# Kernel optimization log

Hardware: AMD Instinct MI355X
Metric: run time of the kernel (lower is better)

## Reference

```python
import jax, jax.numpy as jnp
import numpy as np

def setup_inputs() -> dict:
    key = jax.random.key(0)
    k1, k2, k3, k4, k5 = jax.random.split(key, 5)
    B, Lc, Lq, D = 32, 512, 64, 1024
    return {
        "c": jax.random.normal(k1, (B, Lc, D), dtype=jnp.float32),
        "q": jax.random.normal(k2, (B, Lq, D), dtype=jnp.float32),
        "proj_c": jax.random.normal(k3, (D, 1), dtype=jnp.float32) * 0.04,
        "proj_q": jax.random.normal(k4, (D, 1), dtype=jnp.float32) * 0.04,
        "proj_cq": jax.random.normal(k5, (1, 1, D), dtype=jnp.float32) * 0.04,
    }

def reference(c, q, proj_c, proj_q, proj_cq):
    # similarity: s0 + s1 + s2, shape [B, Lc, Lq]
    s0 = c @ proj_c                                   # [B, Lc, 1]
    s1 = jnp.swapaxes(q @ proj_q, 1, 2)               # [B, 1, Lq]
    s2 = jnp.einsum('bcd,bqd->bcq', c * proj_cq, q)   # [B, Lc, Lq]
    sim = s0 + s1 + s2

    # context-to-query attention
    a_c2q = jax.nn.softmax(sim, axis=-1)              # [B, Lc, Lq]
    c2q = jnp.einsum('bcq,bqd->bcd', a_c2q, q)        # [B, Lc, D]

    # query-to-context attention (max over query dim, softmax over context)
    a_q2c = jax.nn.softmax(jnp.max(sim, axis=-1), axis=-1)  # [B, Lc]
    q2c = jnp.einsum('bc,bcd->bd', a_q2c, c)[:, None, :]    # [B, 1, D], broadcasts over Lc

    out = jnp.concatenate((c, c2q, c * q2c, c * c2q), axis=-1)  # [B, Lc, 4D]
    return out
```

## Files before the change

kernel.cpp:

```cpp
#include <hip/hip_runtime.h>

#define B 32
#define LC 512
#define LQ 64
#define DD 1024


typedef __attribute__((ext_vector_type(8))) short bf16x8;
typedef __attribute__((ext_vector_type(4))) float f32x4;

__device__ inline short f2bf(float f) {
    unsigned u = __builtin_bit_cast(unsigned, f);
    u += 0x7FFFu + ((u >> 16) & 1u);
    return (short)(u >> 16);
}

__device__ inline bf16x8 pack8(float4 a, float4 b) {
    bf16x8 r;
    r[0] = f2bf(a.x); r[1] = f2bf(a.y); r[2] = f2bf(a.z); r[3] = f2bf(a.w);
    r[4] = f2bf(b.x); r[5] = f2bf(b.y); r[6] = f2bf(b.z); r[7] = f2bf(b.w);
    return r;
}

__device__ inline float dot4(float4 a, float4 b) {
    return a.x * b.x + a.y * b.y + a.z * b.z + a.w * b.w;
}

__device__ inline int xswz(int bid, int nwg) {
    return (bid & 7) * (nwg >> 3) + (bid >> 3);
}

__global__ __launch_bounds__(256) void k0_q(const float* __restrict__ q,
                                            const float* __restrict__ proj_q,
                                            short* __restrict__ qbf,
                                            short* __restrict__ qT,
                                            float* __restrict__ s1part) {
    const int bid = xswz(blockIdx.x, 512);
    const int b  = bid >> 4;
    const int d0 = (bid & 15) * 64;
    const int sl = bid & 15;
    const int t  = threadIdx.x;

    __shared__ __align__(16) short tile[64][72];
    __shared__ float s1red[64][8];

    const int j0 = (t & 31) * 2;
    const int dg = t >> 5;

    const float* qr0 = q + (size_t)(b * LQ + j0) * DD + d0 + dg * 8;
    const float* qr1 = qr0 + DD;
    float4 x0 = *(const float4*)(qr0 + 0);
    float4 x1 = *(const float4*)(qr0 + 4);
    float4 y0 = *(const float4*)(qr1 + 0);
    float4 y1 = *(const float4*)(qr1 + 4);
    float4 p0 = *(const float4*)(proj_q + d0 + dg * 8);
    float4 p1 = *(const float4*)(proj_q + d0 + dg * 8 + 4);

    s1red[j0][dg]     = dot4(x0, p0) + dot4(x1, p1);
    s1red[j0 + 1][dg] = dot4(y0, p0) + dot4(y1, p1);

    *(bf16x8*)&qbf[(size_t)(b * LQ + j0) * DD + d0 + dg * 8]     = pack8(x0, x1);
    *(bf16x8*)&qbf[(size_t)(b * LQ + j0 + 1) * DD + d0 + dg * 8] = pack8(y0, y1);

    const float* fx0 = (const float*)&x0;
    const float* fx1 = (const float*)&x1;
    const float* fy0 = (const float*)&y0;
    const float* fy1 = (const float*)&y1;
#pragma unroll
    for (int e = 0; e < 8; ++e) {
        float v0 = (e < 4) ? fx0[e] : fx1[e - 4];
        float v1 = (e < 4) ? fy0[e] : fy1[e - 4];
        unsigned pk = (unsigned)(unsigned short)f2bf(v0)
                    | ((unsigned)(unsigned short)f2bf(v1) << 16);
        *(unsigned*)&tile[dg * 8 + e][j0] = pk;
    }
    __syncthreads();

    {
        const int d = t >> 2, part = t & 3;
        bf16x8 v0 = *(const bf16x8*)&tile[d][part * 16];
        bf16x8 v1 = *(const bf16x8*)&tile[d][part * 16 + 8];
        short* dst = qT + ((size_t)b * DD + d0 + d) * LQ + part * 16;
        *(bf16x8*)(dst)     = v0;
        *(bf16x8*)(dst + 8) = v1;
    }
    if (t < 64) {
        float s = 0.f;
#pragma unroll
        for (int k = 0; k < 8; ++k) s += s1red[t][k];
        s1part[(b * 16 + sl) * 64 + t] = s;
    }
}

__global__ __launch_bounds__(256) void k1_sim(const float* __restrict__ c,
                                              const short* __restrict__ qbf,
                                              const float* __restrict__ proj_c,
                                              const float* __restrict__ proj_cq,
                                              const float* __restrict__ s1part,
                                              short* __restrict__ P,
                                              float* __restrict__ mfull) {
    const int bid = xswz(blockIdx.x, 512);
    const int b  = bid >> 4;
    const int i0 = (bid & 15) * 32;
    const int t  = threadIdx.x;
    const int w  = t >> 6, lane = t & 63;
    const int l15 = lane & 15, quad = lane >> 4;

    __shared__ __align__(16) short sA[32][72];
    __shared__ __align__(16) short sB[64][72];
    __shared__ float rmaxL[32][4];
    __shared__ float rsumL[32][4];
    __shared__ float s0red[32][8];
    __shared__ float s1L[64];

    const int arow = t >> 3, ag = t & 7;
    const int brow = t >> 2, bg = t & 3;

    const float* cbase = c + (size_t)(b * LC + i0 + arow) * DD + ag * 8;
    const short* qbase = qbf + (size_t)(b * LQ + brow) * DD + bg * 16;

    f32x4 acc[2] = {{0.f,0.f,0.f,0.f},{0.f,0.f,0.f,0.f}};
    float s0p = 0.f;

    float4 a0 = *(const float4*)(cbase + 0);
    float4 a1 = *(const float4*)(cbase + 4);
    bf16x8 u0 = *(const bf16x8*)(qbase + 0);
    bf16x8 u1 = *(const bf16x8*)(qbase + 8);

    for (int kc = 0; kc < 16; ++kc) {
        float4 na0, na1;
        bf16x8 nu0, nu1;
        if (kc < 15) {
            const float* cn = cbase + (kc + 1) * 64;
            const short* qn = qbase + (kc + 1) * 64;
            na0 = *(const float4*)(cn + 0);
            na1 = *(const float4*)(cn + 4);
            nu0 = *(const bf16x8*)(qn + 0);
            nu1 = *(const bf16x8*)(qn + 8);
        }
        {
            const float* pcq = proj_cq + kc * 64 + ag * 8;
            const float* pc  = proj_c  + kc * 64 + ag * 8;
            float4 p0 = *(const float4*)(pcq + 0);
            float4 p1 = *(const float4*)(pcq + 4);
            float4 c0 = *(const float4*)(pc + 0);
            float4 c1 = *(const float4*)(pc + 4);
            s0p += dot4(a0, c0) + dot4(a1, c1);
            float4 m0 = {a0.x * p0.x, a0.y * p0.y, a0.z * p0.z, a0.w * p0.w};
            float4 m1 = {a1.x * p1.x, a1.y * p1.y, a1.z * p1.z, a1.w * p1.w};
            *(bf16x8*)&sA[arow][ag * 8] = pack8(m0, m1);
            *(bf16x8*)&sB[brow][bg * 16 + 0] = u0;
            *(bf16x8*)&sB[brow][bg * 16 + 8] = u1;
        }
        __syncthreads();
#pragma unroll
        for (int s = 0; s < 2; ++s) {
            int ko = s * 32 + quad * 8;
            bf16x8 bf = *(const bf16x8*)&sB[w * 16 + l15][ko];
#pragma unroll
            for (int mt = 0; mt < 2; ++mt) {
                bf16x8 af = *(const bf16x8*)&sA[mt * 16 + l15][ko];
                acc[mt] = __builtin_amdgcn_mfma_f32_16x16x32_bf16(af, bf, acc[mt], 0, 0, 0);
            }
        }
        __syncthreads();
        if (kc < 15) { a0 = na0; a1 = na1; u0 = nu0; u1 = nu1; }
    }

    s0red[arow][ag] = s0p;
    if (t < 64) {
        float s = 0.f;
#pragma unroll
        for (int k = 0; k < 16; ++k) s += s1part[(b * 16 + k) * 64 + t];
        s1L[t] = s;
    }
    __syncthreads();

    const float s1j = s1L[w * 16 + l15];
    float v[2][4];
#pragma unroll
    for (int mt = 0; mt < 2; ++mt) {
#pragma unroll
        for (int r = 0; r < 4; ++r) {
            float vv = acc[mt][r] + s1j;
            v[mt][r] = vv;
            float rm = vv;
#pragma unroll
            for (int off = 1; off < 16; off <<= 1) rm = fmaxf(rm, __shfl_xor(rm, off, 16));
            if (l15 == 0) rmaxL[mt * 16 + quad * 4 + r][w] = rm;
        }
    }
    __syncthreads();
    float e[2][4];
#pragma unroll
    for (int mt = 0; mt < 2; ++mt) {
#pragma unroll
        for (int r = 0; r < 4; ++r) {
            int row = mt * 16 + quad * 4 + r;
            float m = fmaxf(fmaxf(rmaxL[row][0], rmaxL[row][1]),
                            fmaxf(rmaxL[row][2], rmaxL[row][3]));
            float ee = __expf(v[mt][r] - m);
            e[mt][r] = ee;
            float se = ee;
#pragma unroll
            for (int off = 1; off < 16; off <<= 1) se += __shfl_xor(se, off, 16);
            if (l15 == 0) rsumL[row][w] = se;
        }
    }
    __syncthreads();
#pragma unroll
    for (int mt = 0; mt < 2; ++mt) {
#pragma unroll
        for (int r = 0; r < 4; ++r) {
            int row = mt * 16 + quad * 4 + r;
            float s = rsumL[row][0] + rsumL[row][1] + rsumL[row][2] + rsumL[row][3];
            P[(size_t)(b * LC + i0 + row) * LQ + w * 16 + l15] = f2bf(e[mt][r] / s);
        }
    }
    if (t < 32) {
        float s0v = 0.f;
#pragma unroll
        for (int k = 0; k < 8; ++k) s0v += s0red[t][k];
        float mm = fmaxf(fmaxf(rmaxL[t][0], rmaxL[t][1]),
                         fmaxf(rmaxL[t][2], rmaxL[t][3]));
        mfull[b * LC + i0 + t] = mm + s0v;
    }
}

__global__ __launch_bounds__(256) void k2_q2c(const float* __restrict__ c,
                                              const float* __restrict__ mfull,
                                              float* __restrict__ q2c) {
    const int bid = xswz(blockIdx.x, 256);
    const int b  = bid >> 3;
    const int d0 = (bid & 7) * 128;
    const int t  = threadIdx.x;
    __shared__ float aL[LC];
    __shared__ float redm[4];
    __shared__ float reds[4];

    float m0 = mfull[b * LC + t];
    float m1 = mfull[b * LC + 256 + t];
    float mx = fmaxf(m0, m1);
#pragma unroll
    for (int off = 32; off; off >>= 1) mx = fmaxf(mx, __shfl_xor(mx, off, 64));
    if ((t & 63) == 0) redm[t >> 6] = mx;
    __syncthreads();
    float bm = fmaxf(fmaxf(redm[0], redm[1]), fmaxf(redm[2], redm[3]));
    float e0 = __expf(m0 - bm), e1 = __expf(m1 - bm);
    float s = e0 + e1;
#pragma unroll
    for (int off = 32; off; off >>= 1) s += __shfl_xor(s, off, 64);
    if ((t & 63) == 0) reds[t >> 6] = s;
    __syncthreads();
    float bs = reds[0] + reds[1] + reds[2] + reds[3];
    float inv = 1.0f / bs;
    aL[t] = e0 * inv;
    aL[t + 256] = e1 * inv;
    __syncthreads();

    const int tx = t & 31, ty = t >> 5;
    float4 acc = {0.f, 0.f, 0.f, 0.f};
    const float* cb = c + (size_t)b * LC * DD + d0 + tx * 4;
    for (int i = ty; i < LC; i += 8) {
        float a = aL[i];
        float4 cv = *(const float4*)(cb + (size_t)i * DD);
        acc.x += a * cv.x; acc.y += a * cv.y; acc.z += a * cv.z; acc.w += a * cv.w;
    }
    __shared__ __align__(16) float4 red[8][32];
    red[ty][tx] = acc;
    __syncthreads();
    if (t < 32) {
        float4 sv = red[0][t];
#pragma unroll
        for (int k = 1; k < 8; ++k) {
            float4 v2 = red[k][t];
            sv.x += v2.x; sv.y += v2.y; sv.z += v2.z; sv.w += v2.w;
        }
        *(float4*)(q2c + b * DD + d0 + t * 4) = sv;
    }
}

__global__ __launch_bounds__(256) void k3_out(const float* __restrict__ c,
                                              const short* __restrict__ qT,
                                              const short* __restrict__ P,
                                              const float* __restrict__ q2c,
                                              float* __restrict__ out) {
    const int bid = xswz(blockIdx.x, 2048);
    const int b  = bid >> 6;
    const int i0 = ((bid >> 2) & 15) * 32;
    const int qd = bid & 3;
    const int t  = threadIdx.x;
    const int w  = t >> 6, lane = t & 63;
    const int l15 = lane & 15, quad = lane >> 4;

    __shared__ __align__(16) short sBq[256][72];

    bf16x8 paf[2][2];
#pragma unroll
    for (int s = 0; s < 2; ++s)
#pragma unroll
        for (int mt = 0; mt < 2; ++mt)
            paf[s][mt] = *(const bf16x8*)&P[(size_t)(b * LC + i0 + mt * 16 + l15) * LQ
                                           + s * 32 + quad * 8];

    {
        const short* src = qT + ((size_t)b * DD + qd * 256) * LQ;
#pragma unroll
        for (int it = 0; it < 8; ++it) {
            int f = it * 256 + t;
            bf16x8 vv = *(const bf16x8*)(src + f * 8);
            *(bf16x8*)&sBq[f >> 3][(f & 7) * 8] = vv;
        }
    }
    __syncthreads();

    const float* cb  = c + (size_t)(b * LC + i0) * DD + qd * 256;
    const float* g2b = q2c + b * DD + qd * 256;
    float* ob = out + (size_t)(b * LC + i0) * (4 * DD) + qd * 256;

    for (int dci = 0; dci < 4; ++dci) {
        const int dl = dci * 64 + w * 16 + l15;
        float g2 = g2b[dl];
        f32x4 acc2[2] = {{0.f,0.f,0.f,0.f},{0.f,0.f,0.f,0.f}};
#pragma unroll
        for (int s = 0; s < 2; ++s) {
            bf16x8 bf = *(const bf16x8*)&sBq[dl][s * 32 + quad * 8];
#pragma unroll
            for (int mt = 0; mt < 2; ++mt)
                acc2[mt] = __builtin_amdgcn_mfma_f32_16x16x32_bf16(paf[s][mt], bf, acc2[mt], 0, 0, 0);
        }
#pragma unroll
        for (int mt = 0; mt < 2; ++mt) {
#pragma unroll
            for (int r = 0; r < 4; ++r) {
                int row = mt * 16 + quad * 4 + r;
                float cc = cb[(size_t)row * DD + dl];
                float cqv = acc2[mt][r];
                float* o = ob + (size_t)row * (4 * DD) + dl;
                o[0]      = cc;
                o[DD]     = cqv;
                o[2 * DD] = cc * g2;
                o[3 * DD] = cc * cqv;
            }
        }
    }
}

extern "C" void kernel_launch(void* const* d_in, const int* in_sizes, int n_in,
                              void* d_out, int out_size, void* d_ws, size_t ws_size,
                              hipStream_t stream) {
    const float* c       = (const float*)d_in[0];
    const float* q       = (const float*)d_in[1];
    const float* proj_c  = (const float*)d_in[2];
    const float* proj_q  = (const float*)d_in[3];
    const float* proj_cq = (const float*)d_in[4];
    float* out = (float*)d_out;
    float* ws  = (float*)d_ws;

    float* mfull  = ws;
    float* q2c    = ws + 16384;
    float* s1part = ws + 49152;
    short* P      = (short*)(ws + 81920);
    short* qbf    = (short*)(ws + 606208);
    short* qT     = (short*)(ws + 1654784);

    hipLaunchKernelGGL(k0_q,   dim3(512),  dim3(256), 0, stream, q, proj_q, qbf, qT, s1part);
    hipLaunchKernelGGL(k1_sim, dim3(512),  dim3(256), 0, stream,
                       c, qbf, proj_c, proj_cq, s1part, P, mfull);
    hipLaunchKernelGGL(k2_q2c, dim3(256),  dim3(256), 0, stream, c, mfull, q2c);
    hipLaunchKernelGGL(k3_out, dim3(2048), dim3(256), 0, stream, c, qT, P, q2c, out);
}
```

Measured before the change: 390.2 us.

## Double-buffer sim kernel, load MFMA B fragments directly, vectorize output stores

In the similarity kernel, the q bf16 B-fragments are now loaded straight from global memory into registers instead of staging them through shared memory. The A tile is double-buffered with a two-step prefetch, so each k-step needs one barrier instead of two. In the output kernel, the shared-memory staging of qT is removed and fragments are read directly from global memory. A 4x4 in-register transpose built from lane shuffles lets each lane issue float4 loads of c and float4 stores of all four output slices instead of scalar accesses. The trade-off is uncoalesced fragment loads from global memory and extra shuffle instructions in return for wider, better-coalesced output writes.

```diff
diff --git a/kernel.cpp b/kernel.cpp
--- a/kernel.cpp
+++ b/kernel.cpp
@@ -28,6 +28,20 @@
 
 __device__ inline int xswz(int bid, int nwg) {
     return (bid & 7) * (nwg >> 3) + (bid >> 3);
+}
+
+__device__ inline void xpose44(float v[4], int l15) {
+    const bool m0 = l15 & 1, m1 = l15 & 2;
+    float x0 = m0 ? v[0] : v[1];
+    float x1 = m0 ? v[2] : v[3];
+    x0 = __shfl_xor(x0, 1, 64);
+    x1 = __shfl_xor(x1, 1, 64);
+    if (m0) { v[0] = x0; v[2] = x1; } else { v[1] = x0; v[3] = x1; }
+    float y0 = m1 ? v[0] : v[2];
+    float y1 = m1 ? v[1] : v[3];
+    y0 = __shfl_xor(y0, 2, 64);
+    y1 = __shfl_xor(y1, 2, 64);
+    if (m1) { v[0] = y0; v[1] = y1; } else { v[2] = y0; v[3] = y1; }
 }
 
 __global__ __launch_bounds__(256) void k0_q(const float* __restrict__ q,
@@ -106,41 +120,64 @@
     const int w  = t >> 6, lane = t & 63;
     const int l15 = lane & 15, quad = lane >> 4;
 
-    __shared__ __align__(16) short sA[32][72];
-    __shared__ __align__(16) short sB[64][72];
+    __shared__ __align__(16) short sA[2][32][72];
     __shared__ float rmaxL[32][4];
     __shared__ float rsumL[32][4];
     __shared__ float s0red[32][8];
     __shared__ float s1L[64];
 
     const int arow = t >> 3, ag = t & 7;
-    const int brow = t >> 2, bg = t & 3;
 
     const float* cbase = c + (size_t)(b * LC + i0 + arow) * DD + ag * 8;
-    const short* qbase = qbf + (size_t)(b * LQ + brow) * DD + bg * 16;
+    const short* qfrag = qbf + (size_t)(b * LQ + w * 16 + l15) * DD + quad * 8;
 
     f32x4 acc[2] = {{0.f,0.f,0.f,0.f},{0.f,0.f,0.f,0.f}};
     float s0p = 0.f;
 
     float4 a0 = *(const float4*)(cbase + 0);
     float4 a1 = *(const float4*)(cbase + 4);
-    bf16x8 u0 = *(const bf16x8*)(qbase + 0);
-    bf16x8 u1 = *(const bf16x8*)(qbase + 8);
+    bf16x8 bcur[2], bnxt[2];
+#pragma unroll
+    for (int s = 0; s < 2; ++s)
+        bcur[s] = *(const bf16x8*)(qfrag + s * 32);
+    {
+        float4 p0 = *(const float4*)(proj_cq + ag * 8);
+        float4 p1 = *(const float4*)(proj_cq + ag * 8 + 4);
+        float4 c0 = *(const float4*)(proj_c + ag * 8);
+        float4 c1 = *(const float4*)(proj_c + ag * 8 + 4);
+        s0p += dot4(a0, c0) + dot4(a1, c1);
+        float4 m0 = {a0.x * p0.x, a0.y * p0.y, a0.z * p0.z, a0.w * p0.w};
+        float4 m1 = {a1.x * p1.x, a1.y * p1.y, a1.z * p1.z, a1.w * p1.w};
+        *(bf16x8*)&sA[0][arow][ag * 8] = pack8(m0, m1);
+    }
+    a0 = *(const float4*)(cbase + 64);
+    a1 = *(const float4*)(cbase + 68);
+    __syncthreads();
 
     for (int kc = 0; kc < 16; ++kc) {
+        const int cur = kc & 1;
         float4 na0, na1;
-        bf16x8 nu0, nu1;
+        if (kc < 14) {
+            na0 = *(const float4*)(cbase + (kc + 2) * 64);
+            na1 = *(const float4*)(cbase + (kc + 2) * 64 + 4);
+        }
         if (kc < 15) {
-            const float* cn = cbase + (kc + 1) * 64;
-            const short* qn = qbase + (kc + 1) * 64;
-            na0 = *(const float4*)(cn + 0);
-            na1 = *(const float4*)(cn + 4);
-            nu0 = *(const bf16x8*)(qn + 0);
-            nu1 = *(const bf16x8*)(qn + 8);
-        }
-        {
-            const float* pcq = proj_cq + kc * 64 + ag * 8;
-            const float* pc  = proj_c  + kc * 64 + ag * 8;
+#pragma unroll
+            for (int s = 0; s < 2; ++s)
+                bnxt[s] = *(const bf16x8*)(qfrag + (kc + 1) * 64 + s * 32);
+        }
+#pragma unroll
+        for (int s = 0; s < 2; ++s) {
+            int ko = s * 32 + quad * 8;
+#pragma unroll
+            for (int mt = 0; mt < 2; ++mt) {
+                bf16x8 af = *(const bf16x8*)&sA[cur][mt * 16 + l15][ko];
+                acc[mt] = __builtin_amdgcn_mfma_f32_16x16x32_bf16(af, bcur[s], acc[mt], 0, 0, 0);
+            }
+        }
+        if (kc < 15) {
+            const float* pcq = proj_cq + (kc + 1) * 64 + ag * 8;
+            const float* pc  = proj_c  + (kc + 1) * 64 + ag * 8;
             float4 p0 = *(const float4*)(pcq + 0);
             float4 p1 = *(const float4*)(pcq + 4);
             float4 c0 = *(const float4*)(pc + 0);
@@ -148,23 +185,11 @@
             s0p += dot4(a0, c0) + dot4(a1, c1);
             float4 m0 = {a0.x * p0.x, a0.y * p0.y, a0.z * p0.z, a0.w * p0.w};
             float4 m1 = {a1.x * p1.x, a1.y * p1.y, a1.z * p1.z, a1.w * p1.w};
-            *(bf16x8*)&sA[arow][ag * 8] = pack8(m0, m1);
-            *(bf16x8*)&sB[brow][bg * 16 + 0] = u0;
-            *(bf16x8*)&sB[brow][bg * 16 + 8] = u1;
+            *(bf16x8*)&sA[cur ^ 1][arow][ag * 8] = pack8(m0, m1);
+            a0 = na0; a1 = na1;
+            bcur[0] = bnxt[0]; bcur[1] = bnxt[1];
         }
         __syncthreads();
-#pragma unroll
-        for (int s = 0; s < 2; ++s) {
-            int ko = s * 32 + quad * 8;
-            bf16x8 bf = *(const bf16x8*)&sB[w * 16 + l15][ko];
-#pragma unroll
-            for (int mt = 0; mt < 2; ++mt) {
-                bf16x8 af = *(const bf16x8*)&sA[mt * 16 + l15][ko];
-                acc[mt] = __builtin_amdgcn_mfma_f32_16x16x32_bf16(af, bf, acc[mt], 0, 0, 0);
-            }
-        }
-        __syncthreads();
-        if (kc < 15) { a0 = na0; a1 = na1; u0 = nu0; u1 = nu1; }
     }
 
     s0red[arow][ag] = s0p;
@@ -293,8 +318,6 @@
     const int w  = t >> 6, lane = t & 63;
     const int l15 = lane & 15, quad = lane >> 4;
 
-    __shared__ __align__(16) short sBq[256][72];
-
     bf16x8 paf[2][2];
 #pragma unroll
     for (int s = 0; s < 2; ++s)
@@ -303,45 +326,38 @@
             paf[s][mt] = *(const bf16x8*)&P[(size_t)(b * LC + i0 + mt * 16 + l15) * LQ
                                            + s * 32 + quad * 8];
 
-    {
-        const short* src = qT + ((size_t)b * DD + qd * 256) * LQ;
-#pragma unroll
-        for (int it = 0; it < 8; ++it) {
-            int f = it * 256 + t;
-            bf16x8 vv = *(const bf16x8*)(src + f * 8);
-            *(bf16x8*)&sBq[f >> 3][(f & 7) * 8] = vv;
-        }
-    }
-    __syncthreads();
-
-    const float* cb  = c + (size_t)(b * LC + i0) * DD + qd * 256;
-    const float* g2b = q2c + b * DD + qd * 256;
-    float* ob = out + (size_t)(b * LC + i0) * (4 * DD) + qd * 256;
+    const short* qTb = qT + ((size_t)b * DD + qd * 256 + w * 16 + l15) * LQ + quad * 8;
 
     for (int dci = 0; dci < 4; ++dci) {
-        const int dl = dci * 64 + w * 16 + l15;
-        float g2 = g2b[dl];
         f32x4 acc2[2] = {{0.f,0.f,0.f,0.f},{0.f,0.f,0.f,0.f}};
 #pragma unroll
         for (int s = 0; s < 2; ++s) {
-            bf16x8 bf = *(const bf16x8*)&sBq[dl][s * 32 + quad * 8];
+            bf16x8 bf = *(const bf16x8*)(qTb + (size_t)dci * 64 * LQ + s * 32);
 #pragma unroll
             for (int mt = 0; mt < 2; ++mt)
                 acc2[mt] = __builtin_amdgcn_mfma_f32_16x16x32_bf16(paf[s][mt], bf, acc2[mt], 0, 0, 0);
         }
+
+        float t0[4] = {acc2[0][0], acc2[0][1], acc2[0][2], acc2[0][3]};
+        float t1[4] = {acc2[1][0], acc2[1][1], acc2[1][2], acc2[1][3]};
+        xpose44(t0, l15);
+        xpose44(t1, l15);
+
+        const int dglob = qd * 256 + dci * 64 + w * 16 + 4 * (l15 >> 2);
+        float4 g2 = *(const float4*)(q2c + b * DD + dglob);
+
 #pragma unroll
         for (int mt = 0; mt < 2; ++mt) {
-#pragma unroll
-            for (int r = 0; r < 4; ++r) {
-                int row = mt * 16 + quad * 4 + r;
-                float cc = cb[(size_t)row * DD + dl];
-                float cqv = acc2[mt][r];
-                float* o = ob + (size_t)row * (4 * DD) + dl;
-                o[0]      = cc;
-                o[DD]     = cqv;
-                o[2 * DD] = cc * g2;
-                o[3 * DD] = cc * cqv;
-            }
+            const int row = i0 + mt * 16 + quad * 4 + (l15 & 3);
+            float4 cqv = mt ? *(float4*)t1 : *(float4*)t0;
+            float4 cc = *(const float4*)(c + (size_t)(b * LC + row) * DD + dglob);
+            float* ob = out + (size_t)(b * LC + row) * (4 * DD) + dglob;
+            *(float4*)(ob) = cc;
+            *(float4*)(ob + DD) = cqv;
+            float4 o2 = {cc.x * g2.x, cc.y * g2.y, cc.z * g2.z, cc.w * g2.w};
+            *(float4*)(ob + 2 * DD) = o2;
+            float4 o3 = {cc.x * cqv.x, cc.y * cqv.y, cc.z * cqv.z, cc.w * cqv.w};
+            *(float4*)(ob + 3 * DD) = o3;
         }
     }
 }
```

Measured after the change: 391.5 us. About the same (+0.3%).

## Restructure output kernel to stage c2q tile in LDS for float4 coalesced stores

Applied to the files above, without the earlier changes.

The output kernel now has each block cover 16 context rows across the full D, instead of 32 rows by a quarter of D. MFMA results for c2q go into an LDS tile, and the c loads and the four output writes are then done as coalesced float4 accesses. Before, each thread wrote scalar floats, one per column, spread across rows. The qT operand is read straight from global memory instead of being staged in LDS. The aim is more efficient writes of the large output tensor, at the cost of extra barriers and redundant qT reads per block.

```diff
diff --git a/kernel.cpp b/kernel.cpp
--- a/kernel.cpp
+++ b/kernel.cpp
@@ -285,64 +285,54 @@
                                               const short* __restrict__ P,
                                               const float* __restrict__ q2c,
                                               float* __restrict__ out) {
-    const int bid = xswz(blockIdx.x, 2048);
-    const int b  = bid >> 6;
-    const int i0 = ((bid >> 2) & 15) * 32;
-    const int qd = bid & 3;
+    const int bid = xswz(blockIdx.x, 1024);
+    const int b  = bid >> 5;
+    const int i0 = (bid & 31) * 16;
     const int t  = threadIdx.x;
     const int w  = t >> 6, lane = t & 63;
     const int l15 = lane & 15, quad = lane >> 4;
 
-    __shared__ __align__(16) short sBq[256][72];
-
-    bf16x8 paf[2][2];
+    __shared__ __align__(16) float ct[16][260];
+
+    bf16x8 paf[2];
 #pragma unroll
     for (int s = 0; s < 2; ++s)
-#pragma unroll
-        for (int mt = 0; mt < 2; ++mt)
-            paf[s][mt] = *(const bf16x8*)&P[(size_t)(b * LC + i0 + mt * 16 + l15) * LQ
-                                           + s * 32 + quad * 8];
-
-    {
-        const short* src = qT + ((size_t)b * DD + qd * 256) * LQ;
-#pragma unroll
-        for (int it = 0; it < 8; ++it) {
-            int f = it * 256 + t;
-            bf16x8 vv = *(const bf16x8*)(src + f * 8);
-            *(bf16x8*)&sBq[f >> 3][(f & 7) * 8] = vv;
-        }
-    }
-    __syncthreads();
-
-    const float* cb  = c + (size_t)(b * LC + i0) * DD + qd * 256;
-    const float* g2b = q2c + b * DD + qd * 256;
-    float* ob = out + (size_t)(b * LC + i0) * (4 * DD) + qd * 256;
-
-    for (int dci = 0; dci < 4; ++dci) {
-        const int dl = dci * 64 + w * 16 + l15;
-        float g2 = g2b[dl];
-        f32x4 acc2[2] = {{0.f,0.f,0.f,0.f},{0.f,0.f,0.f,0.f}};
-#pragma unroll
-        for (int s = 0; s < 2; ++s) {
-            bf16x8 bf = *(const bf16x8*)&sBq[dl][s * 32 + quad * 8];
-#pragma unroll
-            for (int mt = 0; mt < 2; ++mt)
-                acc2[mt] = __builtin_amdgcn_mfma_f32_16x16x32_bf16(paf[s][mt], bf, acc2[mt], 0, 0, 0);
-        }
-#pragma unroll
-        for (int mt = 0; mt < 2; ++mt) {
-#pragma unroll
-            for (int r = 0; r < 4; ++r) {
-                int row = mt * 16 + quad * 4 + r;
-                float cc = cb[(size_t)row * DD + dl];
-                float cqv = acc2[mt][r];
-                float* o = ob + (size_t)row * (4 * DD) + dl;
-                o[0]      = cc;
-                o[DD]     = cqv;
-                o[2 * DD] = cc * g2;
-                o[3 * DD] = cc * cqv;
+        paf[s] = *(const bf16x8*)&P[(size_t)(b * LC + i0 + l15) * LQ + s * 32 + quad * 8];
+
+    const short* qTb = qT + ((size_t)b * DD + w * 16 + l15) * LQ + quad * 8;
+
+    for (int g = 0; g < 4; ++g) {
+#pragma unroll
+        for (int dci = 0; dci < 4; ++dci) {
+            const int dloc = g * 256 + dci * 64;
+            f32x4 acc2 = {0.f, 0.f, 0.f, 0.f};
+#pragma unroll
+            for (int s = 0; s < 2; ++s) {
+                bf16x8 bf = *(const bf16x8*)(qTb + (size_t)dloc * LQ + s * 32);
+                acc2 = __builtin_amdgcn_mfma_f32_16x16x32_bf16(paf[s], bf, acc2, 0, 0, 0);
             }
-        }
+#pragma unroll
+            for (int r = 0; r < 4; ++r)
+                ct[quad * 4 + r][dci * 64 + w * 16 + l15] = acc2[r];
+        }
+        __syncthreads();
+
+        const int dg = g * 256 + lane * 4;
+        float4 g2 = *(const float4*)(q2c + b * DD + dg);
+#pragma unroll
+        for (int k = 0; k < 4; ++k) {
+            const int row = w * 4 + k;
+            float4 cc  = *(const float4*)(c + (size_t)(b * LC + i0 + row) * DD + dg);
+            float4 cqv = *(const float4*)&ct[row][lane * 4];
+            float* ob = out + (size_t)(b * LC + i0 + row) * (4 * DD) + dg;
+            *(float4*)(ob) = cc;
+            *(float4*)(ob + DD) = cqv;
+            float4 o2 = {cc.x * g2.x, cc.y * g2.y, cc.z * g2.z, cc.w * g2.w};
+            *(float4*)(ob + 2 * DD) = o2;
+            float4 o3 = {cc.x * cqv.x, cc.y * cqv.y, cc.z * cqv.z, cc.w * cqv.w};
+            *(float4*)(ob + 3 * DD) = o3;
+        }
+        __syncthreads();
     }
 }
 
@@ -368,5 +358,5 @@
     hipLaunchKernelGGL(k1_sim, dim3(512),  dim3(256), 0, stream,
                        c, qbf, proj_c, proj_cq, s1part, P, mfull);
     hipLaunchKernelGGL(k2_q2c, dim3(256),  dim3(256), 0, stream, c, mfull, q2c);
-    hipLaunchKernelGGL(k3_out, dim3(2048), dim3(256), 0, stream, c, qT, P, q2c, out);
-}
+    hipLaunchKernelGGL(k3_out, dim3(1024), dim3(256), 0, stream, c, qT, P, q2c, out);
+}
```

Result: faster. 373.4 us (-4.3%).
